# Kernel tuning notes

Measured on AMD Instinct MI355X. Metric: run time of the kernel, lower is better.

## Reference

```python
import jax, jax.numpy as jnp
import numpy as np

B, S, D, H = 2, 2048, 1024, 16
DK = D // H


def setup_inputs() -> dict:
    key = jax.random.key(0)
    ks = jax.random.split(key, 12)
    scale = 1.0 / np.sqrt(D)
    inp = {
        "query": jax.random.normal(ks[0], (B, S, D), jnp.float32),
        "key": jax.random.normal(ks[1], (B, S, D), jnp.float32),
        "value": jax.random.normal(ks[2], (B, S, D), jnp.float32),
        "mask": jax.random.randint(ks[3], (B, 1, S, S), 0, 2, jnp.int32),
        "Wq": jax.random.normal(ks[4], (D, D), jnp.float32) * scale,
        "bq": jnp.zeros((D,), jnp.float32),
        "Wk": jax.random.normal(ks[5], (D, D), jnp.float32) * scale,
        "bk": jnp.zeros((D,), jnp.float32),
        "Wv": jax.random.normal(ks[6], (D, D), jnp.float32) * scale,
        "bv": jnp.zeros((D,), jnp.float32),
        "Wo": jax.random.normal(ks[7], (D, D), jnp.float32) * scale,
        "bo": jnp.zeros((D,), jnp.float32),
    }
    return inp


def reference(query, key, value, mask, Wq, bq, Wk, bk, Wv, bv, Wo, bo):
    # Linear projections (dropout is identity in eval mode)
    q = query @ Wq + bq          # (B,S,D)
    k = key @ Wk + bk
    v = value @ Wv + bv

    # split heads: (B,S,D) -> (B,H,S,DK)
    def split(x):
        return x.reshape(B, S, H, DK).transpose(0, 2, 1, 3)

    q, k, v = split(q), split(k), split(v)

    scores = jnp.einsum("bhqd,bhkd->bhqk", q, k) / jnp.sqrt(jnp.float32(DK))
    scores = jnp.where(mask == 0, jnp.float32(-1e9), scores)
    p_attn = jax.nn.softmax(scores, axis=-1)   # (B,H,S,S)

    att = jnp.einsum("bhqk,bhkd->bhqd", p_attn, v)  # (B,H,S,DK)
    merged = att.transpose(0, 2, 1, 3).reshape(B, S, D)
    return merged @ Wo + bo
```

## Files before the change

### kernel.cpp

```cpp
#include <hip/hip_runtime.h>
#include <hip/hip_bf16.h>
#include <cstdint>
#include <cstddef>


#define B_ 2
#define S_ 2048
#define D_ 1024
#define H_ 16
#define M_ 4096

typedef unsigned short u16;
typedef __attribute__((ext_vector_type(8))) short bf16x8;
typedef __attribute__((ext_vector_type(8))) unsigned short u16x8;
typedef __attribute__((ext_vector_type(4))) unsigned short u16x4;
typedef __attribute__((ext_vector_type(4))) unsigned int u32x4;
typedef __attribute__((ext_vector_type(4))) float f32x4;
typedef __attribute__((ext_vector_type(4))) int i32x4;

#define QSCALE 0.18033688011112042f

__device__ __forceinline__ u16 f2bf(float f) {
  __hip_bfloat16 h = __float2bfloat16(f);
  return *reinterpret_cast<u16*>(&h);
}

__device__ __forceinline__ unsigned cvtpk(float lo, float hi) {
  unsigned r;
  asm("v_cvt_pk_bf16_f32 %0, %1, %2" : "=v"(r) : "v"(lo), "v"(hi));
  return r;
}

__device__ __forceinline__ void gload_lds16(const void* g, void* l) {
  __builtin_amdgcn_global_load_lds((const __attribute__((address_space(1))) void*)g,
                                   (__attribute__((address_space(3))) void*)l, 16, 0, 0);
}

__global__ __launch_bounds__(256) void k_convert(const float* __restrict__ q, const float* __restrict__ k,
                                                 const float* __restrict__ v,
                                                 u16* __restrict__ xq, u16* __restrict__ xk, u16* __restrict__ xv) {
  int z = blockIdx.y;
  const float* src = (z == 0) ? q : (z == 1) ? k : v;
  u16* dst = (z == 0) ? xq : (z == 1) ? xk : xv;
  size_t i = ((size_t)blockIdx.x * 256 + threadIdx.x) * 8;
  f32x4 a = *(const f32x4*)(src + i);
  f32x4 b = *(const f32x4*)(src + i + 4);
  u16x8 o;
  o[0]=f2bf(a[0]); o[1]=f2bf(a[1]); o[2]=f2bf(a[2]); o[3]=f2bf(a[3]);
  o[4]=f2bf(b[0]); o[5]=f2bf(b[1]); o[6]=f2bf(b[2]); o[7]=f2bf(b[3]);
  *(u16x8*)(dst + i) = o;
}

__global__ __launch_bounds__(256) void k_transposeW(const float* __restrict__ w0, const float* __restrict__ w1,
                                                    const float* __restrict__ w2, const float* __restrict__ w3,
                                                    u16* __restrict__ t0, u16* __restrict__ t1,
                                                    u16* __restrict__ t2, u16* __restrict__ t3) {
  int z = blockIdx.z;
  const float* W = (z==0)?w0:(z==1)?w1:(z==2)?w2:w3;
  u16* Wt = (z==0)?t0:(z==1)?t1:(z==2)?t2:t3;
  __shared__ float tile[32][33];
  int tx = threadIdx.x & 31, ty = threadIdx.x >> 5;
  int bx = blockIdx.x * 32, by = blockIdx.y * 32;
  #pragma unroll
  for (int p = 0; p < 4; ++p)
    tile[ty + p*8][tx] = W[(size_t)(by + ty + p*8) * D_ + bx + tx];
  __syncthreads();
  #pragma unroll
  for (int p = 0; p < 4; ++p)
    Wt[(size_t)(bx + ty + p*8) * D_ + by + tx] = f2bf(tile[tx][ty + p*8]);
}

__global__ __launch_bounds__(256) void k_packmask(const int* __restrict__ mask, u16* __restrict__ out) {
  size_t t = (size_t)blockIdx.x * 256 + threadIdx.x;
  const int* p = mask + t * 64;
  unsigned wds0 = 0, wds1 = 0, wds2 = 0, wds3 = 0;
  #pragma unroll
  for (int c = 0; c < 16; ++c) {
    i32x4 v = *(const i32x4*)(p + c*4);
    #pragma unroll
    for (int e = 0; e < 4; ++e) {
      const int k = c*4 + e;
      const int lcw = (k >> 3) & 3;
      const int ni = ((k >> 4) & 2) | ((k >> 2) & 1);
      const unsigned bit = 1u << (4*ni + (k & 3));
      if (v[e]) {
        if (lcw == 0) wds0 |= bit; else if (lcw == 1) wds1 |= bit;
        else if (lcw == 2) wds2 |= bit; else wds3 |= bit;
      }
    }
  }
  u16x4 w; w[0] = (u16)wds0; w[1] = (u16)wds1; w[2] = (u16)wds2; w[3] = (u16)wds3;
  *(u16x4*)(out + t*4) = w;
}

template<int CMODE, int MI, int NI>
__device__ __forceinline__ void gemm_core(const u16* __restrict__ A, const u16* __restrict__ Bt,
                                          const float* __restrict__ bias, void* __restrict__ Cv, float scale) {
  __shared__ u16 As[MI*32*64];
  __shared__ u16 Bs[NI*32*64];
  const int t = threadIdx.x;
  const int l = t & 63, w = t >> 6;
  const int wr = w >> 1, wc = w & 1;
  const int lr = l & 15, lc = l >> 4;
  const int bm = blockIdx.x, bn = blockIdx.y;
  f32x4 acc[MI][NI];
  #pragma unroll
  for (int i = 0; i < MI; ++i)
    #pragma unroll
    for (int j = 0; j < NI; ++j) { f32x4 z = {0.f,0.f,0.f,0.f}; acc[i][j] = z; }
  const int srow = t >> 3;
  const u16* ga = A  + (size_t)(bm*(MI*32) + srow) * 1024;
  const u16* gb = Bt + (size_t)(bn*(NI*32) + srow) * 1024;
  u16* la = &As[t*8];
  u16* lb = &Bs[t*8];
  for (int kt = 0; kt < 16; ++kt) {
    const int ko = kt * 64;
    __syncthreads();
    #pragma unroll
    for (int i = 0; i < MI; ++i) {
      int blk = (t & 7) ^ ((i*32 + srow) & 7);
      gload_lds16(ga + (size_t)(i*32)*1024 + ko + blk*8, la + i*2048);
    }
    #pragma unroll
    for (int i = 0; i < NI; ++i) {
      int blk = (t & 7) ^ ((i*32 + srow) & 7);
      gload_lds16(gb + (size_t)(i*32)*1024 + ko + blk*8, lb + i*2048);
    }
    __syncthreads();
    #pragma unroll
    for (int ks = 0; ks < 2; ++ks) {
      bf16x8 af[MI], bfr[NI];
      #pragma unroll
      for (int mi = 0; mi < MI; ++mi)
        af[mi]  = *(const bf16x8*)&As[(wr*(MI*16) + mi*16 + lr)*64 + (((ks*4 + lc) ^ (lr & 7))*8)];
      #pragma unroll
      for (int ni = 0; ni < NI; ++ni)
        bfr[ni] = *(const bf16x8*)&Bs[(wc*(NI*16) + ni*16 + lr)*64 + (((ks*4 + lc) ^ (lr & 7))*8)];
      #pragma unroll
      for (int mi = 0; mi < MI; ++mi)
        #pragma unroll
        for (int ni = 0; ni < NI; ++ni)
          acc[mi][ni] = __builtin_amdgcn_mfma_f32_16x16x32_bf16(af[mi], bfr[ni], acc[mi][ni], 0, 0, 0);
    }
  }
  #pragma unroll
  for (int ni = 0; ni < NI; ++ni) {
    int gcol = bn*(NI*32) + wc*(NI*16) + ni*16 + lr;
    float bv = bias[gcol];
    #pragma unroll
    for (int mi = 0; mi < MI; ++mi) {
      int grow = bm*(MI*32) + wr*(MI*16) + mi*16 + lc*4;
      if (CMODE == 2) {
        u16x4 pk;
        #pragma unroll
        for (int j = 0; j < 4; ++j) pk[j] = f2bf((acc[mi][ni][j] + bv) * scale);
        *(u16x4*)&((u16*)Cv)[(size_t)gcol * M_ + grow] = pk;
      } else {
        #pragma unroll
        for (int j = 0; j < 4; ++j) {
          float v = (acc[mi][ni][j] + bv) * scale;
          if (CMODE == 0) ((u16*)Cv)[(size_t)(grow + j) * 1024 + gcol] = f2bf(v);
          else            ((float*)Cv)[(size_t)(grow + j) * 1024 + gcol] = v;
        }
      }
    }
  }
}

__global__ __launch_bounds__(256) void k_gemm_qkv(const u16* Xq, const u16* Xk, const u16* Xv,
                                                  const u16* Wqt, const u16* Wkt, const u16* Wvt,
                                                  const float* bq, const float* bk, const float* bv,
                                                  u16* Qo, u16* Ko, u16* Vt, float qscale) {
  int z = blockIdx.z;
  if (z == 0)      gemm_core<0,4,4>(Xq, Wqt, bq, Qo, qscale);
  else if (z == 1) gemm_core<0,4,4>(Xk, Wkt, bk, Ko, 1.f);
  else             gemm_core<2,4,4>(Xv, Wvt, bv, Vt, 1.f);
}

__global__ __launch_bounds__(256) void k_gemm_out(const u16* Aatt, const u16* Wot, const float* bo, float* out) {
  gemm_core<1,4,2>(Aatt, Wot, bo, out, 1.f);
}

__global__ __launch_bounds__(512, 8) void k_attn(const u16* __restrict__ Q, const u16* __restrict__ Kb,
                                                 const u16* __restrict__ Vt,
                                                 const u16* __restrict__ mbw,
                                                 u16* __restrict__ attb) {
  __shared__ u16 Ks[3*4096];
  __shared__ u16 Vs[2*4096];
  const int t = threadIdx.x, l = t & 63, w = t >> 6;
  const int lr = l & 15, lc = l >> 4;
  const int qt = blockIdx.x, h = blockIdx.y, b = blockIdx.z;
  const int r0 = t >> 3;
  const int c0 = (t & 7) ^ (r0 & 7);
  const int pr0 = (r0 & 32) | ((r0 & 12) << 1) | ((r0 & 16) >> 2) | (r0 & 3);
  const u16* kp0 = Kb + (size_t)(b*S_ + pr0)*D_ + h*64 + c0*8;
  const u16* vp0 = Vt + (size_t)(h*64 + r0)*M_ + b*S_ + c0*8;

  gload_lds16(Q + (size_t)(b*S_ + qt*128 + r0)*D_      + h*64 + c0*8, &Ks[t*8]);
  gload_lds16(Q + (size_t)(b*S_ + qt*128 + 64 + r0)*D_ + h*64 + c0*8, &Ks[4096 + t*8]);
  __syncthreads();
  const int qrow = w*16 + lr;
  const int sw0 = ((lc     ) ^ (lr & 7)) * 8;
  const int sw1 = ((4 + lc ) ^ (lr & 7)) * 8;
  const int qbuf = (qrow >> 6) * 4096, qrl = (qrow & 63) * 64;
  bf16x8 aq0 = *(const bf16x8*)&Ks[qbuf + qrl + sw0];
  bf16x8 aq1 = *(const bf16x8*)&Ks[qbuf + qrl + sw1];
  __syncthreads();
  gload_lds16(kp0,                  &Ks[t*8]);
  gload_lds16(vp0,                  &Vs[t*8]);
  gload_lds16(kp0 + (size_t)64*D_,  &Ks[4096 + t*8]);

  const short one_bf = (short)0x3F80;
  const bf16x8 onesf = {one_bf,one_bf,one_bf,one_bf,one_bf,one_bf,one_bf,one_bf};
  f32x4 ls = {0.f,0.f,0.f,0.f};
  f32x4 o[4];
  #pragma unroll
  for (int ni = 0; ni < 4; ++ni) { f32x4 z = {0.f,0.f,0.f,0.f}; o[ni] = z; }
  const u16* mptr = mbw + (size_t)(b*S_ + qt*128 + qrow)*128 + lc;

#define AITER(KT, KC, KN, KNN, VC, VN, WAITN)                                          \
  {                                                                                    \
    asm volatile("s_waitcnt vmcnt(" #WAITN ")");                                       \
    __builtin_amdgcn_s_barrier();                                                      \
    __builtin_amdgcn_sched_barrier(0);                                                 \
    unsigned mw = mptr[(KT)*4];                                                        \
    if ((KT) < 31) gload_lds16(vp0 + (size_t)((KT)+1)*64,      &Vs[(VN)*4096 + t*8]);  \
    if ((KT) < 30) gload_lds16(kp0 + (size_t)((KT)+2)*64*D_,   &Ks[(KNN)*4096 + t*8]); \
    f32x4 s[4];                                                                        \
    _Pragma("unroll")                                                                  \
    for (int ni = 0; ni < 4; ++ni) { f32x4 z = {0.f,0.f,0.f,0.f}; s[ni] = z; }         \
    __builtin_amdgcn_s_setprio(1);                                                     \
    _Pragma("unroll")                                                                  \
    for (int ni = 0; ni < 4; ++ni) {                                                   \
      bf16x8 bk0 = *(const bf16x8*)&Ks[(KC)*4096 + (ni*16 + lr)*64 + sw0];             \
      bf16x8 bk1 = *(const bf16x8*)&Ks[(KC)*4096 + (ni*16 + lr)*64 + sw1];             \
      s[ni] = __builtin_amdgcn_mfma_f32_16x16x32_bf16(bk0, aq0, s[ni], 0, 0, 0);       \
      s[ni] = __builtin_amdgcn_mfma_f32_16x16x32_bf16(bk1, aq1, s[ni], 0, 0, 0);       \
    }                                                                                  \
    __builtin_amdgcn_s_setprio(0);                                                     \
    _Pragma("unroll")                                                                  \
    for (int ni = 0; ni < 4; ++ni)                                                     \
      _Pragma("unroll")                                                                \
      for (int j = 0; j < 4; ++j) {                                                    \
        float pv = __builtin_amdgcn_exp2f(s[ni][j]);                                   \
        int bmsk = ((int)(mw << (31 - (4*ni + j)))) >> 31;                             \
        union { float f; int i; } u; u.f = pv; u.i &= bmsk;                            \
        s[ni][j] = u.f;                                                                \
      }                                                                                \
    u32x4 pw0, pw1;                                                                    \
    pw0[0] = cvtpk(s[0][0], s[0][1]); pw0[1] = cvtpk(s[0][2], s[0][3]);                \
    pw0[2] = cvtpk(s[1][0], s[1][1]); pw0[3] = cvtpk(s[1][2], s[1][3]);                \
    pw1[0] = cvtpk(s[2][0], s[2][1]); pw1[1] = cvtpk(s[2][2], s[2][3]);                \
    pw1[2] = cvtpk(s[3][0], s[3][1]); pw1[3] = cvtpk(s[3][2], s[3][3]);                \
    bf16x8 pa0 = __builtin_bit_cast(bf16x8, pw0);                                      \
    bf16x8 pa1 = __builtin_bit_cast(bf16x8, pw1);                                      \
    __builtin_amdgcn_s_setprio(1);                                                     \
    ls = __builtin_amdgcn_mfma_f32_16x16x32_bf16(pa0, onesf, ls, 0, 0, 0);             \
    ls = __builtin_amdgcn_mfma_f32_16x16x32_bf16(pa1, onesf, ls, 0, 0, 0);             \
    _Pragma("unroll")                                                                  \
    for (int ni = 0; ni < 4; ++ni) {                                                   \
      bf16x8 bv0 = *(const bf16x8*)&Vs[(VC)*4096 + (ni*16 + lr)*64 + sw0];             \
      o[ni] = __builtin_amdgcn_mfma_f32_16x16x32_bf16(pa0, bv0, o[ni], 0, 0, 0);       \
    }                                                                                  \
    _Pragma("unroll")                                                                  \
    for (int ni = 0; ni < 4; ++ni) {                                                   \
      bf16x8 bv1 = *(const bf16x8*)&Vs[(VC)*4096 + (ni*16 + lr)*64 + sw1];             \
      o[ni] = __builtin_amdgcn_mfma_f32_16x16x32_bf16(pa1, bv1, o[ni], 0, 0, 0);       \
    }                                                                                  \
    __builtin_amdgcn_s_setprio(0);                                                     \
  }

  for (int kt = 0; kt < 30; kt += 6) {
    AITER(kt+0, 0,1,2, 0,1, 1);
    AITER(kt+1, 1,2,0, 1,0, 1);
    AITER(kt+2, 2,0,1, 0,1, 1);
    AITER(kt+3, 0,1,2, 1,0, 1);
    AITER(kt+4, 1,2,0, 0,1, 1);
    AITER(kt+5, 2,0,1, 1,0, 1);
  }
  AITER(30, 0,1,2, 0,1, 1);
  AITER(31, 1,2,0, 1,0, 0);
#undef AITER

  float rl[4];
  #pragma unroll
  for (int j = 0; j < 4; ++j) rl[j] = 1.f / ls[j];
  #pragma unroll
  for (int ni = 0; ni < 4; ++ni)
    #pragma unroll
    for (int j = 0; j < 4; ++j) {
      int orow = qt*128 + w*16 + lc*4 + j, dcol = ni*16 + lr;
      attb[(size_t)(b*S_ + orow)*D_ + h*64 + dcol] = f2bf(o[ni][j] * rl[j]);
    }
}

extern "C" void kernel_launch(void* const* d_in, const int* in_sizes, int n_in,
                              void* d_out, int out_size, void* d_ws, size_t ws_size,
                              hipStream_t stream) {
  (void)in_sizes; (void)n_in; (void)out_size; (void)ws_size;
  const float* query = (const float*)d_in[0];
  const float* key   = (const float*)d_in[1];
  const float* value = (const float*)d_in[2];
  const int*   mask  = (const int*)d_in[3];
  const float* Wq = (const float*)d_in[4];
  const float* bq = (const float*)d_in[5];
  const float* Wk = (const float*)d_in[6];
  const float* bk = (const float*)d_in[7];
  const float* Wv = (const float*)d_in[8];
  const float* bv = (const float*)d_in[9];
  const float* Wo = (const float*)d_in[10];
  const float* bo = (const float*)d_in[11];
  float* out = (float*)d_out;
  char* ws = (char*)d_ws;
  const size_t MB = 1024 * 1024;
  u16* Xq  = (u16*)(ws + 0*MB);
  u16* Xk  = (u16*)(ws + 8*MB);
  u16* Xv  = (u16*)(ws + 16*MB);
  u16* Wqt = (u16*)(ws + 24*MB);
  u16* Wkt = (u16*)(ws + 26*MB);
  u16* Wvt = (u16*)(ws + 28*MB);
  u16* Wot = (u16*)(ws + 30*MB);
  u16* Qb  = (u16*)(ws + 32*MB);
  u16* Kb  = (u16*)(ws + 40*MB);
  u16* Vtb = (u16*)(ws + 48*MB);
  u16* mbits = (u16*)(ws + 56*MB);
  u16* attb = (u16*)(ws + 0*MB);

  k_convert  <<<dim3(2048, 3),     256, 0, stream>>>(query, key, value, Xq, Xk, Xv);
  k_transposeW<<<dim3(32, 32, 4),  256, 0, stream>>>(Wq, Wk, Wv, Wo, Wqt, Wkt, Wvt, Wot);
  k_packmask <<<dim3(512),         256, 0, stream>>>(mask, mbits);
  k_gemm_qkv <<<dim3(32, 8, 3),    256, 0, stream>>>(Xq, Xk, Xv, Wqt, Wkt, Wvt, bq, bk, bv,
                                                     Qb, Kb, Vtb, QSCALE);
  k_attn     <<<dim3(16, 16, 2),   512, 0, stream>>>(Qb, Kb, Vtb, mbits, attb);
  k_gemm_out <<<dim3(32, 16),      256, 0, stream>>>(attb, Wot, bo, out);
}
```

Measured before the change: 161.9 us.

## Expand mask to bf16 lane masks, halve attention Q tile, remap block order

The mask packer now writes a pre-expanded 32-bit lane mask per key element (0xFFFF per bf16 lane), so the attention loop ANDs packed bf16 probabilities with a vector load instead of extracting bits per element. Attention blocks shrink to 256 threads and 64 query rows, with twice as many blocks and a swizzled block-id mapping that groups neighbouring blocks for K/V cache reuse. GEMM shared memory becomes dynamic and the per-tile swizzle offset is hoisted out of the loop. The expanded mask is much larger to write and to read (reusing workspace at 8MB), which trades extra memory traffic for fewer ALU ops.

```diff
diff --git a/kernel.cpp b/kernel.cpp
--- a/kernel.cpp
+++ b/kernel.cpp
@@ -70,10 +70,10 @@
     Wt[(size_t)(bx + ty + p*8) * D_ + by + tx] = f2bf(tile[tx][ty + p*8]);
 }
 
-__global__ __launch_bounds__(256) void k_packmask(const int* __restrict__ mask, u16* __restrict__ out) {
+__global__ __launch_bounds__(256) void k_packmask(const int* __restrict__ mask, unsigned* __restrict__ emask) {
   size_t t = (size_t)blockIdx.x * 256 + threadIdx.x;
   const int* p = mask + t * 64;
-  unsigned wds0 = 0, wds1 = 0, wds2 = 0, wds3 = 0;
+  unsigned wds[4] = {0u,0u,0u,0u};
   #pragma unroll
   for (int c = 0; c < 16; ++c) {
     i32x4 v = *(const i32x4*)(p + c*4);
@@ -82,22 +82,32 @@
       const int k = c*4 + e;
       const int lcw = (k >> 3) & 3;
       const int ni = ((k >> 4) & 2) | ((k >> 2) & 1);
-      const unsigned bit = 1u << (4*ni + (k & 3));
-      if (v[e]) {
-        if (lcw == 0) wds0 |= bit; else if (lcw == 1) wds1 |= bit;
-        else if (lcw == 2) wds2 |= bit; else wds3 |= bit;
-      }
-    }
-  }
-  u16x4 w; w[0] = (u16)wds0; w[1] = (u16)wds1; w[2] = (u16)wds2; w[3] = (u16)wds3;
-  *(u16x4*)(out + t*4) = w;
+      if (v[e]) wds[lcw] |= 1u << (4*ni + (k & 3));
+    }
+  }
+  unsigned* o = emask + t * 32;
+  #pragma unroll
+  for (int lc = 0; lc < 4; ++lc) {
+    u32x4 e0, e1;
+    #pragma unroll
+    for (int wd = 0; wd < 4; ++wd) {
+      e0[wd] = (((wds[lc] >> (2*wd)) & 1u)   ? 0x0000FFFFu : 0u)
+             | (((wds[lc] >> (2*wd+1)) & 1u) ? 0xFFFF0000u : 0u);
+      e1[wd] = (((wds[lc] >> (8+2*wd)) & 1u)   ? 0x0000FFFFu : 0u)
+             | (((wds[lc] >> (8+2*wd+1)) & 1u) ? 0xFFFF0000u : 0u);
+    }
+    *(u32x4*)(o + lc*8)     = e0;
+    *(u32x4*)(o + lc*8 + 4) = e1;
+  }
 }
 
 template<int CMODE, int MI, int NI>
 __device__ __forceinline__ void gemm_core(const u16* __restrict__ A, const u16* __restrict__ Bt,
                                           const float* __restrict__ bias, void* __restrict__ Cv, float scale) {
-  __shared__ u16 As[MI*32*64];
-  __shared__ u16 Bs[NI*32*64];
+  extern __shared__ u16 sm[];
+  constexpr int ASZ = MI*32*64;
+  u16* As = sm;
+  u16* Bs = sm + ASZ;
   const int t = threadIdx.x;
   const int l = t & 63, w = t >> 6;
   const int wr = w >> 1, wc = w & 1;
@@ -109,23 +119,18 @@
     #pragma unroll
     for (int j = 0; j < NI; ++j) { f32x4 z = {0.f,0.f,0.f,0.f}; acc[i][j] = z; }
   const int srow = t >> 3;
-  const u16* ga = A  + (size_t)(bm*(MI*32) + srow) * 1024;
-  const u16* gb = Bt + (size_t)(bn*(NI*32) + srow) * 1024;
-  u16* la = &As[t*8];
-  u16* lb = &Bs[t*8];
+  const int blkx = (t & 7) ^ (srow & 7);
+  const u16* ga = A  + (size_t)(bm*(MI*32) + srow)*1024 + blkx*8;
+  const u16* gb = Bt + (size_t)(bn*(NI*32) + srow)*1024 + blkx*8;
   for (int kt = 0; kt < 16; ++kt) {
     const int ko = kt * 64;
     __syncthreads();
     #pragma unroll
-    for (int i = 0; i < MI; ++i) {
-      int blk = (t & 7) ^ ((i*32 + srow) & 7);
-      gload_lds16(ga + (size_t)(i*32)*1024 + ko + blk*8, la + i*2048);
-    }
-    #pragma unroll
-    for (int i = 0; i < NI; ++i) {
-      int blk = (t & 7) ^ ((i*32 + srow) & 7);
-      gload_lds16(gb + (size_t)(i*32)*1024 + ko + blk*8, lb + i*2048);
-    }
+    for (int i = 0; i < MI; ++i)
+      gload_lds16(ga + (size_t)(i*32)*1024 + ko, &As[i*2048 + t*8]);
+    #pragma unroll
+    for (int i = 0; i < NI; ++i)
+      gload_lds16(gb + (size_t)(i*32)*1024 + ko, &Bs[i*2048 + t*8]);
     __syncthreads();
     #pragma unroll
     for (int ks = 0; ks < 2; ++ks) {
@@ -181,34 +186,38 @@
   gemm_core<1,4,2>(Aatt, Wot, bo, out, 1.f);
 }
 
-__global__ __launch_bounds__(512, 8) void k_attn(const u16* __restrict__ Q, const u16* __restrict__ Kb,
-                                                 const u16* __restrict__ Vt,
-                                                 const u16* __restrict__ mbw,
-                                                 u16* __restrict__ attb) {
+__global__ __launch_bounds__(256) void k_attn(const u16* __restrict__ Q, const u16* __restrict__ Kb,
+                                              const u16* __restrict__ Vt,
+                                              const unsigned* __restrict__ emask,
+                                              u16* __restrict__ attb) {
   __shared__ u16 Ks[3*4096];
   __shared__ u16 Vs[2*4096];
   const int t = threadIdx.x, l = t & 63, w = t >> 6;
   const int lr = l & 15, lc = l >> 4;
-  const int qt = blockIdx.x, h = blockIdx.y, b = blockIdx.z;
+  const int id = blockIdx.x + (blockIdx.y << 5) + (blockIdx.z << 9);
+  const int lg = (id & 7) * 128 + (id >> 3);
+  const int qt = lg & 31, h = (lg >> 5) & 15, b = lg >> 9;
   const int r0 = t >> 3;
   const int c0 = (t & 7) ^ (r0 & 7);
-  const int pr0 = (r0 & 32) | ((r0 & 12) << 1) | ((r0 & 16) >> 2) | (r0 & 3);
+  const int pr0 = ((r0 & 12) << 1) | ((r0 & 16) >> 2) | (r0 & 3);
   const u16* kp0 = Kb + (size_t)(b*S_ + pr0)*D_ + h*64 + c0*8;
   const u16* vp0 = Vt + (size_t)(h*64 + r0)*M_ + b*S_ + c0*8;
 
-  gload_lds16(Q + (size_t)(b*S_ + qt*128 + r0)*D_      + h*64 + c0*8, &Ks[t*8]);
-  gload_lds16(Q + (size_t)(b*S_ + qt*128 + 64 + r0)*D_ + h*64 + c0*8, &Ks[4096 + t*8]);
+  gload_lds16(Q + (size_t)(b*S_ + qt*64 + r0)*D_      + h*64 + c0*8, &Ks[t*8]);
+  gload_lds16(Q + (size_t)(b*S_ + qt*64 + r0 + 32)*D_ + h*64 + c0*8, &Ks[2048 + t*8]);
   __syncthreads();
   const int qrow = w*16 + lr;
   const int sw0 = ((lc     ) ^ (lr & 7)) * 8;
   const int sw1 = ((4 + lc ) ^ (lr & 7)) * 8;
-  const int qbuf = (qrow >> 6) * 4096, qrl = (qrow & 63) * 64;
-  bf16x8 aq0 = *(const bf16x8*)&Ks[qbuf + qrl + sw0];
-  bf16x8 aq1 = *(const bf16x8*)&Ks[qbuf + qrl + sw1];
+  bf16x8 aq0 = *(const bf16x8*)&Ks[qrow*64 + sw0];
+  bf16x8 aq1 = *(const bf16x8*)&Ks[qrow*64 + sw1];
   __syncthreads();
-  gload_lds16(kp0,                  &Ks[t*8]);
-  gload_lds16(vp0,                  &Vs[t*8]);
-  gload_lds16(kp0 + (size_t)64*D_,  &Ks[4096 + t*8]);
+  gload_lds16(kp0,                                 &Ks[t*8]);
+  gload_lds16(kp0 + (size_t)32*D_,                 &Ks[2048 + t*8]);
+  gload_lds16(vp0,                                 &Vs[t*8]);
+  gload_lds16(vp0 + (size_t)32*M_,                 &Vs[2048 + t*8]);
+  gload_lds16(kp0 + (size_t)64*D_,                 &Ks[4096 + t*8]);
+  gload_lds16(kp0 + (size_t)64*D_ + (size_t)32*D_, &Ks[4096 + 2048 + t*8]);
 
   const short one_bf = (short)0x3F80;
   const bf16x8 onesf = {one_bf,one_bf,one_bf,one_bf,one_bf,one_bf,one_bf,one_bf};
@@ -216,16 +225,26 @@
   f32x4 o[4];
   #pragma unroll
   for (int ni = 0; ni < 4; ++ni) { f32x4 z = {0.f,0.f,0.f,0.f}; o[ni] = z; }
-  const u16* mptr = mbw + (size_t)(b*S_ + qt*128 + qrow)*128 + lc;
-
-#define AITER(KT, KC, KN, KNN, VC, VN, WAITN)                                          \
-  {                                                                                    \
+  const unsigned* mkp = emask + (size_t)(b*S_ + qt*64 + qrow)*1024 + lc*8;
+  const u16* vpA = vp0;
+  const u16* vpB = vp0 + (size_t)32*M_;
+  const u16* kpA = kp0;
+  const u16* kpB = kp0 + (size_t)32*D_;
+
+#define AITER(N, KC, VC, VN, KNN, KPRE, VPRE, WAITN) {                                 \
     asm volatile("s_waitcnt vmcnt(" #WAITN ")");                                       \
     __builtin_amdgcn_s_barrier();                                                      \
     __builtin_amdgcn_sched_barrier(0);                                                 \
-    unsigned mw = mptr[(KT)*4];                                                        \
-    if ((KT) < 31) gload_lds16(vp0 + (size_t)((KT)+1)*64,      &Vs[(VN)*4096 + t*8]);  \
-    if ((KT) < 30) gload_lds16(kp0 + (size_t)((KT)+2)*64*D_,   &Ks[(KNN)*4096 + t*8]); \
+    u32x4 mk0 = *(const u32x4*)(mkp + (N)*32);                                         \
+    u32x4 mk1 = *(const u32x4*)(mkp + (N)*32 + 4);                                     \
+    if (VPRE) {                                                                        \
+      gload_lds16(vpA + ((N)+1)*64, &Vs[(VN)*4096 + t*8]);                             \
+      gload_lds16(vpB + ((N)+1)*64, &Vs[(VN)*4096 + 2048 + t*8]);                      \
+    }                                                                                  \
+    if (KPRE) {                                                                        \
+      gload_lds16(kpA + (size_t)((N)+2)*64*D_, &Ks[(KNN)*4096 + t*8]);                 \
+      gload_lds16(kpB + (size_t)((N)+2)*64*D_, &Ks[(KNN)*4096 + 2048 + t*8]);          \
+    }                                                                                  \
     f32x4 s[4];                                                                        \
     _Pragma("unroll")                                                                  \
     for (int ni = 0; ni < 4; ++ni) { f32x4 z = {0.f,0.f,0.f,0.f}; s[ni] = z; }         \
@@ -241,17 +260,15 @@
     _Pragma("unroll")                                                                  \
     for (int ni = 0; ni < 4; ++ni)                                                     \
       _Pragma("unroll")                                                                \
-      for (int j = 0; j < 4; ++j) {                                                    \
-        float pv = __builtin_amdgcn_exp2f(s[ni][j]);                                   \
-        int bmsk = ((int)(mw << (31 - (4*ni + j)))) >> 31;                             \
-        union { float f; int i; } u; u.f = pv; u.i &= bmsk;                            \
-        s[ni][j] = u.f;                                                                \
-      }                                                                                \
+      for (int j = 0; j < 4; ++j)                                                      \
+        s[ni][j] = __builtin_amdgcn_exp2f(s[ni][j]);                                   \
     u32x4 pw0, pw1;                                                                    \
     pw0[0] = cvtpk(s[0][0], s[0][1]); pw0[1] = cvtpk(s[0][2], s[0][3]);                \
     pw0[2] = cvtpk(s[1][0], s[1][1]); pw0[3] = cvtpk(s[1][2], s[1][3]);                \
     pw1[0] = cvtpk(s[2][0], s[2][1]); pw1[1] = cvtpk(s[2][2], s[2][3]);                \
     pw1[2] = cvtpk(s[3][0], s[3][1]); pw1[3] = cvtpk(s[3][2], s[3][3]);                \
+    pw0 &= mk0;                                                                        \
+    pw1 &= mk1;                                                                        \
     bf16x8 pa0 = __builtin_bit_cast(bf16x8, pw0);                                      \
     bf16x8 pa1 = __builtin_bit_cast(bf16x8, pw1);                                      \
     __builtin_amdgcn_s_setprio(1);                                                     \
@@ -270,16 +287,19 @@
     __builtin_amdgcn_s_setprio(0);                                                     \
   }
 
-  for (int kt = 0; kt < 30; kt += 6) {
-    AITER(kt+0, 0,1,2, 0,1, 1);
-    AITER(kt+1, 1,2,0, 1,0, 1);
-    AITER(kt+2, 2,0,1, 0,1, 1);
-    AITER(kt+3, 0,1,2, 1,0, 1);
-    AITER(kt+4, 1,2,0, 0,1, 1);
-    AITER(kt+5, 2,0,1, 1,0, 1);
-  }
-  AITER(30, 0,1,2, 0,1, 1);
-  AITER(31, 1,2,0, 1,0, 0);
+  for (int it = 0; it < 5; ++it) {
+    AITER(0, 0,0, 1,2, 1,1, 2);
+    AITER(1, 1,1, 0,0, 1,1, 2);
+    AITER(2, 2,0, 1,1, 1,1, 2);
+    AITER(3, 0,1, 0,2, 1,1, 2);
+    AITER(4, 1,0, 1,0, 1,1, 2);
+    AITER(5, 2,1, 0,1, 1,1, 2);
+    mkp += 6*32;
+    vpA += 6*64;            vpB += 6*64;
+    kpA += (size_t)6*64*D_; kpB += (size_t)6*64*D_;
+  }
+  AITER(0, 0,0, 1,0, 0,1, 2);
+  AITER(1, 1,1, 0,0, 0,0, 0);
 #undef AITER
 
   float rl[4];
@@ -289,7 +309,7 @@
   for (int ni = 0; ni < 4; ++ni)
     #pragma unroll
     for (int j = 0; j < 4; ++j) {
-      int orow = qt*128 + w*16 + lc*4 + j, dcol = ni*16 + lr;
+      int orow = qt*64 + w*16 + lc*4 + j, dcol = ni*16 + lr;
       attb[(size_t)(b*S_ + orow)*D_ + h*64 + dcol] = f2bf(o[ni][j] * rl[j]);
     }
 }
@@ -323,14 +343,14 @@
   u16* Qb  = (u16*)(ws + 32*MB);
   u16* Kb  = (u16*)(ws + 40*MB);
   u16* Vtb = (u16*)(ws + 48*MB);
-  u16* mbits = (u16*)(ws + 56*MB);
+  unsigned* emask = (unsigned*)(ws + 8*MB);
   u16* attb = (u16*)(ws + 0*MB);
 
-  k_convert  <<<dim3(2048, 3),     256, 0, stream>>>(query, key, value, Xq, Xk, Xv);
-  k_transposeW<<<dim3(32, 32, 4),  256, 0, stream>>>(Wq, Wk, Wv, Wo, Wqt, Wkt, Wvt, Wot);
-  k_packmask <<<dim3(512),         256, 0, stream>>>(mask, mbits);
-  k_gemm_qkv <<<dim3(32, 8, 3),    256, 0, stream>>>(Xq, Xk, Xv, Wqt, Wkt, Wvt, bq, bk, bv,
-                                                     Qb, Kb, Vtb, QSCALE);
-  k_attn     <<<dim3(16, 16, 2),   512, 0, stream>>>(Qb, Kb, Vtb, mbits, attb);
-  k_gemm_out <<<dim3(32, 16),      256, 0, stream>>>(attb, Wot, bo, out);
-}
+  k_convert  <<<dim3(2048, 3),     256, 0,     stream>>>(query, key, value, Xq, Xk, Xv);
+  k_transposeW<<<dim3(32, 32, 4),  256, 0,     stream>>>(Wq, Wk, Wv, Wo, Wqt, Wkt, Wvt, Wot);
+  k_gemm_qkv <<<dim3(32, 8, 3),    256, 32768, stream>>>(Xq, Xk, Xv, Wqt, Wkt, Wvt, bq, bk, bv,
+                                                         Qb, Kb, Vtb, QSCALE);
+  k_packmask <<<dim3(512),         256, 0,     stream>>>(mask, emask);
+  k_attn     <<<dim3(32, 16, 2),   256, 0,     stream>>>(Qb, Kb, Vtb, emask, attb);
+  k_gemm_out <<<dim3(32, 16),      256, 24576, stream>>>(attb, Wot, bo, out);
+}
```

Measured after the change: 151.1 us. -6.7%, faster.
